# Kernel tuning notes

Hardware: AMD Instinct MI355X
Metric: run time of the kernel (lower is better)

Reference implementation:

```python
import jax, jax.numpy as jnp
import numpy as np

N_NODES = 100000
N_EDGES = 500000
HIDDEN = 32
HEADS = 4
PROJ = HIDDEN * HEADS  # 128
LN_EPS = 1e-5


def setup_inputs() -> dict:
    key = jax.random.key(0)
    ks = jax.random.split(key, 12)
    # Xavier-uniform bound for Linear(3, PROJ): sqrt(6/(3+PROJ))
    b_qkv = float(np.sqrt(6.0 / (3 + PROJ)))
    b_out = float(np.sqrt(6.0 / (PROJ + HIDDEN)))
    return {
        "positions": jax.random.normal(ks[0], (N_NODES, 3), dtype=jnp.float32),
        "edge_index": jax.random.randint(ks[1], (2, N_EDGES), 0, N_NODES, dtype=jnp.int64),
        "Wq": jax.random.uniform(ks[2], (3, PROJ), jnp.float32, -b_qkv, b_qkv),
        "bq": jnp.zeros((PROJ,), jnp.float32),
        "Wk": jax.random.uniform(ks[3], (3, PROJ), jnp.float32, -b_qkv, b_qkv),
        "bk": jnp.zeros((PROJ,), jnp.float32),
        "Wv": jax.random.uniform(ks[4], (3, PROJ), jnp.float32, -b_qkv, b_qkv),
        "bv": jnp.zeros((PROJ,), jnp.float32),
        "Wout": jax.random.uniform(ks[5], (PROJ, HIDDEN), jnp.float32, -b_out, b_out),
        "bout": jnp.zeros((HIDDEN,), jnp.float32),
        "gamma": jnp.ones((HIDDEN,), jnp.float32),
        "beta": jnp.zeros((HIDDEN,), jnp.float32),
    }


def reference(positions, edge_index, Wq, bq, Wk, bk, Wv, bv, Wout, bout, gamma, beta):
    row, col = edge_index[0], edge_index[1]
    rel = positions[row] - positions[col]                      # [E, 3]
    E = rel.shape[0]
    q = (rel @ Wq + bq).reshape(E, HEADS, HIDDEN)              # [E, H, D]
    k = (rel @ Wk + bk).reshape(E, HEADS, HIDDEN)
    v = (rel @ Wv + bv).reshape(E, HEADS, HIDDEN)
    # attention score per (edge, head), softmax over heads
    scores = jnp.sum(q * k, axis=-1) / jnp.sqrt(jnp.float32(HIDDEN))  # [E, H]
    attn = jax.nn.softmax(scores, axis=-1)                     # dropout is identity in eval
    wv = (attn[..., None] * v).reshape(E, PROJ)                # [E, H*D]
    # scatter-mean over destination nodes (col), dim_size = N
    seg_sum = jax.ops.segment_sum(wv, col, num_segments=N_NODES)
    counts = jax.ops.segment_sum(jnp.ones((E,), wv.dtype), col, num_segments=N_NODES)
    mean = seg_sum / jnp.maximum(counts, 1.0)[:, None]         # [N, H*D]
    out = mean @ Wout + bout                                   # [N, D]
    mu = jnp.mean(out, axis=-1, keepdims=True)
    var = jnp.var(out, axis=-1, keepdims=True)
    out = (out - mu) / jnp.sqrt(var + LN_EPS) * gamma + beta
    return jax.nn.silu(out)
```

## Files before the change

### kernel.cpp

```cpp
#include <hip/hip_runtime.h>
#include <hip/hip_bf16.h>
#include <hip/hip_fp16.h>

#define LN_EPS 1e-5f

typedef _Float16 f16x2 __attribute__((ext_vector_type(2)));

__device__ __forceinline__ void pk_atomic_add(_Float16* p, float v0, float v1) {
  f16x2 v;
  v.x = (_Float16)v0;
  v.y = (_Float16)v1;
#if __has_builtin(__builtin_amdgcn_flat_atomic_fadd_v2f16)
  __builtin_amdgcn_flat_atomic_fadd_v2f16((f16x2*)p, v);
#else
  unsafeAtomicAdd((__half2*)p, *(__half2*)&v);
#endif
}


__global__ void precompute_kernel(const float* __restrict__ Wq,
                                  const float* __restrict__ bq,
                                  const float* __restrict__ Wk,
                                  const float* __restrict__ bk,
                                  const float* __restrict__ Wv,
                                  const float* __restrict__ bv,
                                  const float* __restrict__ Wout,
                                  const int* __restrict__ ei,
                                  float* __restrict__ flag,
                                  float* __restrict__ coef,
                                  float* __restrict__ T) {
  __shared__ float sM[4][3][32];
  __shared__ float sCv[4][32];
  int t = threadIdx.x;
  const float scale = 0.17677669529663687f;

  if (t == 0) {
    int all_zero = 1;
    for (int i = 0; i < 8; ++i) all_zero &= (ei[2 * i + 1] == 0);
    flag[0] = all_zero ? 1.0f : 0.0f;
  }

  {
    int h = t >> 5, o = t & 31;
    float m0 = 0, m1 = 0, m2 = 0, cv = 0;
    for (int d = 0; d < 32; ++d) {
      int j = h * 32 + d;
      float w = Wout[j * 32 + o];
      m0 += Wv[0 * 128 + j] * w;
      m1 += Wv[1 * 128 + j] * w;
      m2 += Wv[2 * 128 + j] * w;
      cv += bv[j] * w;
    }
    sM[h][0][o] = m0;
    sM[h][1][o] = m1;
    sM[h][2][o] = m2;
    sCv[h][o] = cv;
  }

  if (t < 40) {
    int h = t / 10, j = t % 10;
    float acc = 0;
    for (int d = 0; d < 32; ++d) {
      int idx = h * 32 + d;
      float q0 = Wq[0 * 128 + idx], q1 = Wq[1 * 128 + idx], q2 = Wq[2 * 128 + idx];
      float k0 = Wk[0 * 128 + idx], k1 = Wk[1 * 128 + idx], k2 = Wk[2 * 128 + idx];
      float bqv = bq[idx], bkv = bk[idx];
      float v;
      switch (j) {
        case 0: v = q0 * k0; break;
        case 1: v = q1 * k1; break;
        case 2: v = q2 * k2; break;
        case 3: v = q0 * k1 + q1 * k0; break;
        case 4: v = q0 * k2 + q2 * k0; break;
        case 5: v = q1 * k2 + q2 * k1; break;
        case 6: v = q0 * bkv + k0 * bqv; break;
        case 7: v = q1 * bkv + k1 * bqv; break;
        case 8: v = q2 * bkv + k2 * bqv; break;
        default: v = bqv * bkv; break;
      }
      acc += v;
    }
    coef[h * 10 + j] = acc * scale;
  }

  __syncthreads();

  for (int idx = t; idx < 512; idx += 128) {
    int j = idx >> 5, col = idx & 31;
    float v;
    if (j < 3)        v = sCv[j][col] - sCv[3][col];
    else if (j < 6)   v = sM[3][j - 3][col];
    else if (j < 15)  { int h = (j - 6) / 3, i = (j - 6) % 3; v = sM[h][i][col] - sM[3][i][col]; }
    else              v = sCv[3][col];
    T[idx] = v;
  }
}

__device__ __forceinline__ void sel_comp(int comp, int& pa, int& pr) {
  if (comp < 3)       { pa = comp;           pr = 3; }
  else if (comp < 6)  { pa = 3;              pr = comp - 3; }
  else if (comp < 15) { pa = (comp - 6) / 3; pr = (comp - 6) % 3; }
  else                { pa = 3;              pr = 3; }
}

__global__ void edge_kernel(const float* __restrict__ pos,
                            const int* __restrict__ ei, int E,
                            const float* __restrict__ flag,
                            const float* __restrict__ coef,
                            _Float16* __restrict__ fsums) {
  const int lane = threadIdx.x & 31;
  const int group = (blockIdx.x * blockDim.x + threadIdx.x) >> 5;
  const int base = group * 32;
  if (base >= E) return;

  const int i64 = (flag[0] != 0.0f) ? 1 : 0;
  const int valid_n = min(32, E - base);
  const int e = base + lane;

  int c = 0;
  float rx = 0, ry = 0, rz = 0, a0 = 0, a1 = 0, a2 = 0;
  if (lane < valid_n) {
    int r, cc;
    if (i64) {
      r = ei[2 * (size_t)e];
      cc = ei[2 * ((size_t)E + e)];
    } else {
      r = ei[e];
      cc = ei[E + e];
    }
    c = cc;
    rx = pos[r * 3 + 0] - pos[cc * 3 + 0];
    ry = pos[r * 3 + 1] - pos[cc * 3 + 1];
    rz = pos[r * 3 + 2] - pos[cc * 3 + 2];
    float s[4];
#pragma unroll
    for (int h = 0; h < 4; ++h) {
      const float* cf = coef + h * 10;
      s[h] = cf[9] + rx * cf[6] + ry * cf[7] + rz * cf[8] + rx * rx * cf[0] +
             ry * ry * cf[1] + rz * rz * cf[2] + rx * ry * cf[3] +
             rx * rz * cf[4] + ry * rz * cf[5];
    }
    float mx = fmaxf(fmaxf(s[0], s[1]), fmaxf(s[2], s[3]));
    float e0 = __expf(s[0] - mx), e1 = __expf(s[1] - mx);
    float e2 = __expf(s[2] - mx), e3 = __expf(s[3] - mx);
    float inv = 1.0f / (e0 + e1 + e2 + e3);
    a0 = e0 * inv; a1 = e1 * inv; a2 = e2 * inv;
  }

  const int pair = lane & 7;
  const int sub  = lane >> 3;
  int pa0, pr0, pa1, pr1;
  sel_comp(2 * pair, pa0, pr0);
  sel_comp(2 * pair + 1, pa1, pr1);

  for (int t2 = 0; t2 < valid_n; t2 += 4) {
    const int src = t2 + sub;
    float tx = __shfl(rx, src, 32);
    float ty = __shfl(ry, src, 32);
    float tz = __shfl(rz, src, 32);
    float b0 = __shfl(a0, src, 32);
    float b1 = __shfl(a1, src, 32);
    float b2 = __shfl(a2, src, 32);
    int   ct = __shfl(c,  src, 32);
    float A0 = (pa0 == 0) ? b0 : (pa0 == 1) ? b1 : (pa0 == 2) ? b2 : 1.0f;
    float R0 = (pr0 == 0) ? tx : (pr0 == 1) ? ty : (pr0 == 2) ? tz : 1.0f;
    float A1 = (pa1 == 0) ? b0 : (pa1 == 1) ? b1 : (pa1 == 2) ? b2 : 1.0f;
    float R1 = (pr1 == 0) ? tx : (pr1 == 1) ? ty : (pr1 == 2) ? tz : 1.0f;
    if (src < valid_n)
      pk_atomic_add(fsums + (size_t)ct * 16 + 2 * pair, A0 * R0, A1 * R1);
  }
}

__global__ void node_kernel(const _Float16* __restrict__ fsums,
                            const float* __restrict__ T,
                            const float* __restrict__ bout,
                            const float* __restrict__ gamma,
                            const float* __restrict__ beta,
                            float* __restrict__ out, int N) {
  int tid = blockIdx.x * blockDim.x + threadIdx.x;
  int node = tid >> 5;
  int col = tid & 31;
  if (node >= N) return;

  float myf = (float)fsums[(size_t)node * 16 + (col & 15)];
  float cnt = __shfl(myf, 15, 32);
  float invc = 1.0f / fmaxf(cnt, 1.0f);

  float acc = bout[col];
#pragma unroll
  for (int j = 0; j < 16; ++j) {
    float fj = __shfl(myf, j, 32);
    acc = fmaf(fj * invc, T[j * 32 + col], acc);
  }

  float sx = acc, sx2 = acc * acc;
#pragma unroll
  for (int off = 16; off >= 1; off >>= 1) {
    sx += __shfl_xor(sx, off);
    sx2 += __shfl_xor(sx2, off);
  }
  float mu = sx * (1.0f / 32.0f);
  float var = sx2 * (1.0f / 32.0f) - mu * mu;
  float inv = rsqrtf(var + LN_EPS);
  float y = (acc - mu) * inv * gamma[col] + beta[col];
  float o = y * (1.0f / (1.0f + __expf(-y)));
  out[(size_t)node * 32 + col] = o;
}

extern "C" void kernel_launch(void* const* d_in, const int* in_sizes, int n_in,
                              void* d_out, int out_size, void* d_ws, size_t ws_size,
                              hipStream_t stream) {
  const float* pos  = (const float*)d_in[0];
  const int*   ei   = (const int*)d_in[1];
  const float* Wq   = (const float*)d_in[2];
  const float* bq   = (const float*)d_in[3];
  const float* Wk   = (const float*)d_in[4];
  const float* bk   = (const float*)d_in[5];
  const float* Wv   = (const float*)d_in[6];
  const float* bv   = (const float*)d_in[7];
  const float* Wout = (const float*)d_in[8];
  const float* bout = (const float*)d_in[9];
  const float* gam  = (const float*)d_in[10];
  const float* bet  = (const float*)d_in[11];

  const int N = in_sizes[0] / 3;
  const int E = in_sizes[1] / 2;

  _Float16* fsums = (_Float16*)d_ws;
  float* tail = (float*)((char*)d_ws + (size_t)N * 32);
  float* flag = tail;
  float* coef = flag + 8;
  float* T    = coef + 40;

  hipMemsetAsync(d_ws, 0, (size_t)N * 16 * sizeof(_Float16), stream);

  precompute_kernel<<<1, 128, 0, stream>>>(Wq, bq, Wk, bk, Wv, bv, Wout, ei,
                                           flag, coef, T);

  int edge_blocks = (E + 255) / 256;
  edge_kernel<<<edge_blocks, 256, 0, stream>>>(pos, ei, E, flag, coef, fsums);

  int node_blocks = (int)(((size_t)N * 32 + 255) / 256);
  node_kernel<<<node_blocks, 256, 0, stream>>>(fsums, T, bout, gam, bet,
                                               (float*)d_out, N);

  (void)n_in; (void)out_size; (void)ws_size;
}
```

Before: 144.7 us.

## Replicate fp16 scatter accumulators per XCD to keep atomics local

Each XCD now scatters into its own replica of the fp16 per-node accumulator buffer, chosen from the hardware XCC_ID register, and the atomic is issued as a raw global_atomic_pk_add_f16. The node kernel sums the 8 replicas before normalising. The aim is to avoid cross-XCD coherence traffic and contention on atomics. In exchange the memset and the node-kernel reads are 8x larger, and correctness relies on XCC_ID being in 0..7.

Measured after the change: 149.3 us. 1.03x slower.

```diff
diff --git a/kernel.cpp b/kernel.cpp
--- a/kernel.cpp
+++ b/kernel.cpp
@@ -3,18 +3,21 @@
 #include <hip/hip_fp16.h>
 
 #define LN_EPS 1e-5f
+#define NREP 8
 
 typedef _Float16 f16x2 __attribute__((ext_vector_type(2)));
 
-__device__ __forceinline__ void pk_atomic_add(_Float16* p, float v0, float v1) {
+__device__ __forceinline__ void pk_atomic_add_xcd(_Float16* p, float v0, float v1) {
   f16x2 v;
   v.x = (_Float16)v0;
   v.y = (_Float16)v1;
-#if __has_builtin(__builtin_amdgcn_flat_atomic_fadd_v2f16)
-  __builtin_amdgcn_flat_atomic_fadd_v2f16((f16x2*)p, v);
-#else
-  unsafeAtomicAdd((__half2*)p, *(__half2*)&v);
-#endif
+  asm volatile("global_atomic_pk_add_f16 %0, %1, off" :: "v"(p), "v"(v) : "memory");
+}
+
+__device__ __forceinline__ int xcc_id() {
+  int x;
+  asm volatile("s_getreg_b32 %0, hwreg(HW_REG_XCC_ID)" : "=s"(x));
+  return x & (NREP - 1);
 }
 
 
@@ -104,7 +107,7 @@
 }
 
 __global__ void edge_kernel(const float* __restrict__ pos,
-                            const int* __restrict__ ei, int E,
+                            const int* __restrict__ ei, int E, int N,
                             const float* __restrict__ flag,
                             const float* __restrict__ coef,
                             _Float16* __restrict__ fsums) {
@@ -112,6 +115,8 @@
   const int group = (blockIdx.x * blockDim.x + threadIdx.x) >> 5;
   const int base = group * 32;
   if (base >= E) return;
+
+  _Float16* frep = fsums + (size_t)xcc_id() * N * 16;
 
   const int i64 = (flag[0] != 0.0f) ? 1 : 0;
   const int valid_n = min(32, E - base);
@@ -167,7 +172,7 @@
     float A1 = (pa1 == 0) ? b0 : (pa1 == 1) ? b1 : (pa1 == 2) ? b2 : 1.0f;
     float R1 = (pr1 == 0) ? tx : (pr1 == 1) ? ty : (pr1 == 2) ? tz : 1.0f;
     if (src < valid_n)
-      pk_atomic_add(fsums + (size_t)ct * 16 + 2 * pair, A0 * R0, A1 * R1);
+      pk_atomic_add_xcd(frep + (size_t)ct * 16 + 2 * pair, A0 * R0, A1 * R1);
   }
 }
 
@@ -182,7 +187,13 @@
   int col = tid & 31;
   if (node >= N) return;
 
-  float myf = (float)fsums[(size_t)node * 16 + (col & 15)];
+  const size_t rep_stride = (size_t)N * 16;
+  const size_t idx = (size_t)node * 16 + (col & 15);
+  float myf = 0.0f;
+#pragma unroll
+  for (int rep = 0; rep < NREP; ++rep)
+    myf += (float)fsums[rep * rep_stride + idx];
+
   float cnt = __shfl(myf, 15, 32);
   float invc = 1.0f / fmaxf(cnt, 1.0f);
 
@@ -227,18 +238,18 @@
   const int E = in_sizes[1] / 2;
 
   _Float16* fsums = (_Float16*)d_ws;
-  float* tail = (float*)((char*)d_ws + (size_t)N * 32);
+  float* tail = (float*)((char*)d_ws + (size_t)NREP * N * 32);
   float* flag = tail;
   float* coef = flag + 8;
   float* T    = coef + 40;
 
-  hipMemsetAsync(d_ws, 0, (size_t)N * 16 * sizeof(_Float16), stream);
+  hipMemsetAsync(d_ws, 0, (size_t)NREP * N * 16 * sizeof(_Float16), stream);
 
   precompute_kernel<<<1, 128, 0, stream>>>(Wq, bq, Wk, bk, Wv, bv, Wout, ei,
                                            flag, coef, T);
 
   int edge_blocks = (E + 255) / 256;
-  edge_kernel<<<edge_blocks, 256, 0, stream>>>(pos, ei, E, flag, coef, fsums);
+  edge_kernel<<<edge_blocks, 256, 0, stream>>>(pos, ei, E, N, flag, coef, fsums);
 
   int node_blocks = (int)(((size_t)N * 32 + 255) / 256);
   node_kernel<<<node_blocks, 256, 0, stream>>>(fsums, T, bout, gam, bet,
```
